# Optimization experiments

Hardware: AMD Instinct MI355X
Metric: run time of the kernel (lower is better)

Reference implementation:

```python
import jax, jax.numpy as jnp
import numpy as np

B, S, H, N, L = 256, 64, 512, 16, 2
OUT_BITS = 32            # ceil(log2(n)), n = 2**32
PTR_BITS = 6             # ceil(log2(seq_len)), seq_len = 64
OUT_DIM = 3 + PTR_BITS   # = 9
T = 2 * OUT_BITS - 1     # 63 sequential decode steps


def _ln(x, g, b):
    m = jnp.mean(x, -1, keepdims=True)
    v = jnp.mean((x - m) ** 2, -1, keepdims=True)
    return (x - m) * jax.lax.rsqrt(v + 1e-5) * g + b


def _s4_step(A, Bm, Cm, D, oW, ob, s, x):
    # diagonal-SSM S4 block step: s (B,H,N) recurrent state, x (B,H) input
    s2 = A * s + Bm * x[:, :, None]
    y = jnp.einsum('bhn,hn->bh', s2, Cm) + D * x
    y = jax.nn.gelu(y, approximate=False) @ oW + ob
    return s2, y


def _forward(input_seq, in_W, in_b, A, Bm, Cm, D, outW, outb, ln_g, ln_b, head_W, head_b):
    Bsz = input_seq.shape[0]
    dt = input_seq.dtype
    x = input_seq @ in_W + in_b            # (B,S,H)
    encoded = x                            # encoded_inputs saved before S4 stack
    # ---- encoder: L S4 blocks, residual + layernorm ----
    for j in range(L):
        def step(s, xt, j=j):
            return _s4_step(A[j], Bm[j], Cm[j], D[j], outW[j], outb[j], s, xt)
        s0 = jnp.zeros((Bsz, H, N), dt)
        _, ys = jax.lax.scan(step, s0, jnp.swapaxes(x, 0, 1))
        x = _ln(jnp.swapaxes(ys, 0, 1) + x, ln_g[j], ln_b[j])
    dec0 = jnp.broadcast_to(jnp.array([0.0, 0.0, 1.0], dt), (Bsz, 3))
    carry0 = (jnp.zeros((L, Bsz, H, N), dt), jnp.zeros((Bsz, H), dt), dec0)
    ones1 = jnp.ones((Bsz, 1), dt)

    def dstep(carry, i):
        states, ctx, dec_in = carry
        dp = dec_in @ in_W + in_b          # (B,H)
        xd = dp
        new_states = []
        for j in range(L):
            s2, y = _s4_step(A[j], Bm[j], Cm[j], D[j], outW[j], outb[j], states[j], xd)
            new_states.append(s2)
            res = jnp.where(i == 0, dp, y)   # torch code: residual=proj on step 0, else doubles x_dec
            xd = _ln(y + res, ln_g[j], ln_b[j])
        is_out = (i % 2) == 0
        # pointer retrieval (only applied on odd steps via where)
        o_ptr = jax.nn.sigmoid((xd + ctx) @ head_W + head_b)
        ptr = jnp.argmax(o_ptr[:, 3:3 + PTR_BITS], axis=1)            # (B,)
        ptr_vec = jnp.take_along_axis(encoded, ptr[:, None, None], axis=1)[:, 0]
        ctx = jnp.where(is_out, ctx, ctx + ptr_vec)
        out = jax.nn.sigmoid((xd + ctx) @ head_W + head_b)            # (B,OUT_DIM)
        next_char = jnp.where(is_out, (out[:, 0:1] > 0.5).astype(dt), jnp.zeros((Bsz, 1), dt))
        tag0 = jnp.where(is_out, 1.0, 0.0) * ones1
        tag1 = ones1 - tag0
        dec_next = jnp.concatenate([next_char, tag0, tag1], axis=1)   # (B,3)
        return (jnp.stack(new_states), ctx, dec_next), out

    _, outs = jax.lax.scan(dstep, carry0, jnp.arange(T))
    return jnp.swapaxes(outs, 0, 1)        # (B, T, OUT_DIM)


def setup_inputs() -> dict:
    ks = jax.random.split(jax.random.key(0), 8)
    f32 = jnp.float32
    return {
        'input_seq': jax.random.uniform(ks[0], (B, S, 3), f32),
        'autoregressive_steps': T,
        'in_W': jax.random.normal(ks[1], (3, H), f32) * 0.5,
        'in_b': jnp.zeros((H,), f32),
        'A': jax.random.uniform(ks[2], (L, H, N), f32, 0.5, 0.99),
        'Bm': jax.random.normal(ks[3], (L, H, N), f32) * 0.1,
        'Cm': jax.random.normal(ks[4], (L, H, N), f32) * 0.1,
        'D': jnp.ones((L, H), f32),
        'outW': jax.random.normal(ks[5], (L, H, H), f32) * 0.02,
        'outb': jnp.zeros((L, H), f32),
        'ln_g': jnp.ones((L, H), f32),
        'ln_b': jnp.zeros((L, H), f32),
        'head_W': jax.random.normal(ks[6], (H, OUT_DIM), f32) * 0.05,
        'head_b': jnp.zeros((OUT_DIM,), f32),
    }


def reference(input_seq, autoregressive_steps, in_W, in_b, A, Bm, Cm, D, outW, outb, ln_g, ln_b, head_W, head_b):
    return _forward(input_seq, in_W, in_b, A, Bm, Cm, D, outW, outb, ln_g, ln_b, head_W, head_b)
```

## Files before the change

### kernel.cpp

```cpp
#include <hip/hip_runtime.h>
#include <math.h>

#define HDIM   512
#define NDIM   16
#define SEQ    64
#define TSTEPS 63
#define BATCH  256
#define ODIM   9
#define NTHR   512


__device__ __forceinline__ float gelu_f32(float x) {
    return 0.5f * x * (1.0f + erff(x * 0.70710678118654752440f));
}

__device__ __forceinline__ float sig32(float x) {
    return 1.0f / (1.0f + expf(-x));
}

__device__ __forceinline__ void load3_l2(const float* p0, const float* p1,
                                         const float* p2,
                                         float& v0, float& v1, float& v2) {
    asm volatile(
        "global_load_dword %0, %3, off sc0\n\t"
        "global_load_dword %1, %4, off sc0\n\t"
        "global_load_dword %2, %5, off sc0\n\t"
        "s_waitcnt vmcnt(0)"
        : "=&v"(v0), "=&v"(v1), "=&v"(v2)
        : "v"(p0), "v"(p1), "v"(p2)
        : "memory");
}
__device__ __forceinline__ float load1_l2(const float* p) {
    float v;
    asm volatile("global_load_dword %0, %1, off sc0\n\t"
                 "s_waitcnt vmcnt(0)"
                 : "=v"(v) : "v"(p) : "memory");
    return v;
}

__global__ __launch_bounds__(NTHR, 2)
void s4_decode_kernel(
    const float* __restrict__ input_seq,
    const float* __restrict__ in_W,
    const float* __restrict__ in_b,
    const float* __restrict__ Aarr,
    const float* __restrict__ Barr,
    const float* __restrict__ Carr,
    const float* __restrict__ Darr,
    const float* __restrict__ outW,
    const float* __restrict__ outb,
    const float* __restrict__ ln_g,
    const float* __restrict__ ln_b,
    const float* __restrict__ headW,
    const float* __restrict__ headb,
    float* __restrict__ out,
    float* gws, float* zws,
    unsigned* fg, unsigned* fz,
    unsigned* fx, unsigned* xid)
{
    __shared__ float  ld_xd[HDIM];
    __shared__ float  ld_gall[4 * HDIM];
    __shared__ float4 ld_z4[16 * 4 * 32];
    __shared__ float  ld_D0[HDIM];
    __shared__ float  ld_D1[HDIM];
    __shared__ float  ld_red[16];
    __shared__ float  ld_hred[8 * ODIM];
    __shared__ float  ld_logit[ODIM + 1];
    __shared__ float  ld_dec[4];
    __shared__ int    ld_ptr;
    __shared__ int    ld_fast;

    const int b    = blockIdx.x;
    const int tid  = threadIdx.x;
    const int hg   = tid >> 4;
    const int n    = tid & 15;
    const int mem  = (b >> 3) & 3;
    const int gbase = b - 8 * mem;
    const int c4   = tid & 31;
    const int rg   = tid >> 5;
    const int rgE  = (rg + ((b * 5) & 15)) & 15;
    const int base_row = rgE * 32;
    const int j0 = 0 + (0 >= mem), j1 = 1 + (1 >= mem), j2 = 2 + (2 >= mem);

    unsigned myxcd;
    asm volatile("s_getreg_b32 %0, hwreg(HW_REG_XCC_ID)" : "=s"(myxcd));
    if (tid == 0) {
        __hip_atomic_store(&xid[b], myxcd, __ATOMIC_RELAXED, __HIP_MEMORY_SCOPE_AGENT);
        __hip_atomic_store(&fx[b], 1u, __ATOMIC_RELEASE, __HIP_MEMORY_SCOPE_AGENT);
        unsigned ok = 1;
        #pragma unroll
        for (int j = 0; j < 4; ++j) {
            if (j == mem) continue;
            while (__hip_atomic_load(&fx[gbase + 8 * j],
                                     __ATOMIC_ACQUIRE, __HIP_MEMORY_SCOPE_AGENT) == 0)
                __builtin_amdgcn_s_sleep(1);
            ok &= (__hip_atomic_load(&xid[gbase + 8 * j],
                                     __ATOMIC_RELAXED, __HIP_MEMORY_SCOPE_AGENT) == myxcd);
        }
        ld_fast = (int)ok;
    }

    float s0[16], s1[16];
    float A0[16], B0[16], C0[16], A1[16], B1[16], C1[16];
    #pragma unroll
    for (int k = 0; k < 16; ++k) {
        int h  = hg + 32 * k;
        int i0 = h * NDIM + n;
        int i1 = (HDIM + h) * NDIM + n;
        A0[k] = Aarr[i0]; B0[k] = Barr[i0]; C0[k] = Carr[i0];
        A1[k] = Aarr[i1]; B1[k] = Barr[i1]; C1[k] = Carr[i1];
        s0[k] = 0.f; s1[k] = 0.f;
    }

    const float inb_t = in_b[tid];
    const float w0 = in_W[tid], w1 = in_W[HDIM + tid], w2 = in_W[2 * HDIM + tid];
    const float ob0 = outb[tid], ob1 = outb[HDIM + tid];
    const float lg0 = ln_g[tid], lg1 = ln_g[HDIM + tid];
    const float lb0 = ln_b[tid], lb1 = ln_b[HDIM + tid];

    ld_D0[tid] = Darr[tid];
    ld_D1[tid] = Darr[HDIM + tid];

    const float4* Wsl = (const float4*)outW + mem * 32 + c4;

    float ctxr = 0.f;
    if (tid == 0) { ld_dec[0] = 0.f; ld_dec[1] = 0.f; ld_dec[2] = 1.f; }
    __syncthreads();
    const bool fast = (ld_fast != 0);

    for (int i = 0; i < TSTEPS; ++i) {
        float dpv = fmaf(ld_dec[0], w0, fmaf(ld_dec[1], w1, fmaf(ld_dec[2], w2, inb_t)));
        __syncthreads();
        ld_xd[tid] = dpv;
        __syncthreads();

        #pragma unroll 1
        for (int blk = 0; blk < 2; ++blk) {
            const unsigned seq = (unsigned)(2 * i + blk + 1);
            {
                float* s  = blk ? s1 : s0;
                float* Ar = blk ? A1 : A0;
                float* Br = blk ? B1 : B0;
                float* Cr = blk ? C1 : C0;
                const float* Dl = blk ? ld_D1 : ld_D0;
                #pragma unroll
                for (int k = 0; k < 16; ++k) {
                    int h = hg + 32 * k;
                    float xh = ld_xd[h];
                    float sv = fmaf(Ar[k], s[k], Br[k] * xh);
                    s[k] = sv;
                    float p = sv * Cr[k];
                    p += __shfl_xor(p, 1);
                    p += __shfl_xor(p, 2);
                    p += __shfl_xor(p, 4);
                    p += __shfl_xor(p, 8);
                    if (n == 0) ld_gall[mem * HDIM + h] = gelu_f32(p + Dl[h] * xh);
                }
            }
            __syncthreads();
            if (fast) {
                gws[b * HDIM + tid] = ld_gall[mem * HDIM + tid];
            } else {
                __hip_atomic_store(&gws[b * HDIM + tid], ld_gall[mem * HDIM + tid],
                                   __ATOMIC_RELAXED, __HIP_MEMORY_SCOPE_AGENT);
            }
            __syncthreads();
            if (tid == 4)
                __hip_atomic_store(&fg[b], seq, __ATOMIC_RELAXED, __HIP_MEMORY_SCOPE_AGENT);
            if (tid < 3) {
                int j = tid + (tid >= mem ? 1 : 0);
                while (__hip_atomic_load(&fg[gbase + 8 * j],
                                         __ATOMIC_RELAXED, __HIP_MEMORY_SCOPE_AGENT) < seq)
                    __builtin_amdgcn_s_sleep(1);
            }
            __syncthreads();
            if (fast) {
                float v0, v1, v2;
                load3_l2(&gws[(gbase + 8 * j0) * HDIM + tid],
                         &gws[(gbase + 8 * j1) * HDIM + tid],
                         &gws[(gbase + 8 * j2) * HDIM + tid], v0, v1, v2);
                ld_gall[j0 * HDIM + tid] = v0;
                ld_gall[j1 * HDIM + tid] = v1;
                ld_gall[j2 * HDIM + tid] = v2;
            } else {
                ld_gall[j0 * HDIM + tid] =
                    __hip_atomic_load(&gws[(gbase + 8 * j0) * HDIM + tid],
                                      __ATOMIC_RELAXED, __HIP_MEMORY_SCOPE_AGENT);
                ld_gall[j1 * HDIM + tid] =
                    __hip_atomic_load(&gws[(gbase + 8 * j1) * HDIM + tid],
                                      __ATOMIC_RELAXED, __HIP_MEMORY_SCOPE_AGENT);
                ld_gall[j2 * HDIM + tid] =
                    __hip_atomic_load(&gws[(gbase + 8 * j2) * HDIM + tid],
                                      __ATOMIC_RELAXED, __HIP_MEMORY_SCOPE_AGENT);
            }
            __syncthreads();
            {
                const float4* Wb = Wsl + (size_t)blk * HDIM * 128;
                float4 acc[4];
                #pragma unroll
                for (int bi = 0; bi < 4; ++bi) acc[bi] = make_float4(0.f, 0.f, 0.f, 0.f);
                float4 a0 = Wb[(size_t)(base_row)     * 128];
                float4 a1 = Wb[(size_t)(base_row + 1) * 128];
                #pragma unroll 2
                for (int rr = 0; rr < 32; rr += 4) {
                    int rB = base_row + ((rr + 2) & 31);
                    float4 b0 = Wb[(size_t)rB * 128];
                    float4 b1 = Wb[(size_t)(rB + 1) * 128];
                    {
                        int r = base_row + rr;
                        #pragma unroll
                        for (int bi = 0; bi < 4; ++bi) {
                            float g0 = ld_gall[bi * HDIM + r];
                            float g1 = ld_gall[bi * HDIM + r + 1];
                            acc[bi].x = fmaf(g1, a1.x, fmaf(g0, a0.x, acc[bi].x));
                            acc[bi].y = fmaf(g1, a1.y, fmaf(g0, a0.y, acc[bi].y));
                            acc[bi].z = fmaf(g1, a1.z, fmaf(g0, a0.z, acc[bi].z));
                            acc[bi].w = fmaf(g1, a1.w, fmaf(g0, a0.w, acc[bi].w));
                        }
                    }
                    int rA = base_row + ((rr + 4) & 31);
                    a0 = Wb[(size_t)rA * 128];
                    a1 = Wb[(size_t)(rA + 1) * 128];
                    {
                        int r = base_row + rr + 2;
                        #pragma unroll
                        for (int bi = 0; bi < 4; ++bi) {
                            float g0 = ld_gall[bi * HDIM + r];
                            float g1 = ld_gall[bi * HDIM + r + 1];
                            acc[bi].x = fmaf(g1, b1.x, fmaf(g0, b0.x, acc[bi].x));
                            acc[bi].y = fmaf(g1, b1.y, fmaf(g0, b0.y, acc[bi].y));
                            acc[bi].z = fmaf(g1, b1.z, fmaf(g0, b0.z, acc[bi].z));
                            acc[bi].w = fmaf(g1, b1.w, fmaf(g0, b0.w, acc[bi].w));
                        }
                    }
                }
                #pragma unroll
                for (int bi = 0; bi < 4; ++bi)
                    ld_z4[(rg * 4 + bi) * 32 + c4] = acc[bi];
            }
            __syncthreads();
            {
                const float* zf = (const float*)ld_z4;
                int bi2 = tid >> 7;
                int col = tid & 127;
                float zv = 0.f;
                #pragma unroll
                for (int k = 0; k < 16; ++k) zv += zf[(k * 4 + bi2) * 128 + col];
                float* zp = &zws[(gbase + 8 * bi2) * HDIM + mem * 128 + col];
                if (fast) *zp = zv;
                else __hip_atomic_store(zp, zv, __ATOMIC_RELAXED, __HIP_MEMORY_SCOPE_AGENT);
            }
            __syncthreads();
            if (tid == 4)
                __hip_atomic_store(&fz[b], seq, __ATOMIC_RELAXED, __HIP_MEMORY_SCOPE_AGENT);
            if (tid < 3) {
                int j = tid + (tid >= mem ? 1 : 0);
                while (__hip_atomic_load(&fz[gbase + 8 * j],
                                         __ATOMIC_RELAXED, __HIP_MEMORY_SCOPE_AGENT) < seq)
                    __builtin_amdgcn_s_sleep(1);
            }
            __syncthreads();
            {
                float zraw = fast ? load1_l2(&zws[b * HDIM + tid])
                                  : __hip_atomic_load(&zws[b * HDIM + tid],
                                                      __ATOMIC_RELAXED,
                                                      __HIP_MEMORY_SCOPE_AGENT);
                float z = zraw + (blk ? ob1 : ob0);
                float res = (i == 0) ? dpv : z;
                float tmp = z + res;
                float v1 = tmp, v2 = tmp * tmp;
                #pragma unroll
                for (int m = 1; m < 64; m <<= 1) {
                    v1 += __shfl_xor(v1, m);
                    v2 += __shfl_xor(v2, m);
                }
                if ((tid & 63) == 0) {
                    ld_red[2 * (tid >> 6)]     = v1;
                    ld_red[2 * (tid >> 6) + 1] = v2;
                }
                __syncthreads();
                float s1r = 0.f, s2r = 0.f;
                #pragma unroll
                for (int q = 0; q < 8; ++q) { s1r += ld_red[2*q]; s2r += ld_red[2*q+1]; }
                float mu  = s1r * (1.f / 512.f);
                float var = s2r * (1.f / 512.f) - mu * mu;
                float rs  = rsqrtf(var + 1e-5f);
                __syncthreads();
                ld_xd[tid] = (tmp - mu) * rs * (blk ? lg1 : lg0) + (blk ? lb1 : lb0);
                __syncthreads();
            }
        }

        {
            float v = ld_xd[tid] + ctxr;
            const float* w = headW + tid * ODIM;
            float p[ODIM];
            #pragma unroll
            for (int o = 0; o < ODIM; ++o) p[o] = v * w[o];
            #pragma unroll
            for (int m = 1; m < 64; m <<= 1) {
                #pragma unroll
                for (int o = 0; o < ODIM; ++o) p[o] += __shfl_xor(p[o], m);
            }
            if ((tid & 63) == 0) {
                int wv = tid >> 6;
                #pragma unroll
                for (int o = 0; o < ODIM; ++o) ld_hred[wv * ODIM + o] = p[o];
            }
            __syncthreads();
            if (tid < ODIM) {
                float s = headb[tid];
                #pragma unroll
                for (int wv = 0; wv < 8; ++wv) s += ld_hred[wv * ODIM + tid];
                ld_logit[tid] = s;
            }
            __syncthreads();
        }

        const bool is_out = ((i & 1) == 0);
        if (is_out) {
            if (tid < ODIM)
                out[(b * TSTEPS + i) * ODIM + tid] = sig32(ld_logit[tid]);
            if (tid == 0) {
                float nc = (sig32(ld_logit[0]) > 0.5f) ? 1.f : 0.f;
                ld_dec[0] = nc; ld_dec[1] = 1.f; ld_dec[2] = 0.f;
            }
            __syncthreads();
        } else {
            if (tid == 0) {
                int best = 0; float bv = sig32(ld_logit[3]);
                #pragma unroll
                for (int o = 1; o < 6; ++o) {
                    float v2 = sig32(ld_logit[3 + o]);
                    if (v2 > bv) { bv = v2; best = o; }
                }
                ld_ptr = best;
                ld_dec[0] = 0.f; ld_dec[1] = 0.f; ld_dec[2] = 1.f;
            }
            __syncthreads();
            {
                const float* iseq = input_seq + (b * SEQ + ld_ptr) * 3;
                float e0 = iseq[0], e1 = iseq[1], e2 = iseq[2];
                ctxr += fmaf(e0, w0, fmaf(e1, w1, fmaf(e2, w2, inb_t)));
            }
            __syncthreads();
            {
                float v = ld_xd[tid] + ctxr;
                const float* w = headW + tid * ODIM;
                float p[ODIM];
                #pragma unroll
                for (int o = 0; o < ODIM; ++o) p[o] = v * w[o];
                #pragma unroll
                for (int m = 1; m < 64; m <<= 1) {
                    #pragma unroll
                    for (int o = 0; o < ODIM; ++o) p[o] += __shfl_xor(p[o], m);
                }
                if ((tid & 63) == 0) {
                    int wv = tid >> 6;
                    #pragma unroll
                    for (int o = 0; o < ODIM; ++o) ld_hred[wv * ODIM + o] = p[o];
                }
                __syncthreads();
                if (tid < ODIM) {
                    float s = headb[tid];
                    #pragma unroll
                    for (int wv = 0; wv < 8; ++wv) s += ld_hred[wv * ODIM + tid];
                    out[(b * TSTEPS + i) * ODIM + tid] = sig32(s);
                }
            }
            __syncthreads();
        }
    }
}

extern "C" void kernel_launch(void* const* d_in, const int* in_sizes, int n_in,
                              void* d_out, int out_size, void* d_ws, size_t ws_size,
                              hipStream_t stream) {
    (void)in_sizes; (void)n_in; (void)ws_size; (void)out_size;
    const float* input_seq = (const float*)d_in[0];
    const float* in_W   = (const float*)d_in[2];
    const float* in_b   = (const float*)d_in[3];
    const float* Aarr   = (const float*)d_in[4];
    const float* Barr   = (const float*)d_in[5];
    const float* Carr   = (const float*)d_in[6];
    const float* Darr   = (const float*)d_in[7];
    const float* outW   = (const float*)d_in[8];
    const float* outb   = (const float*)d_in[9];
    const float* ln_g   = (const float*)d_in[10];
    const float* ln_b   = (const float*)d_in[11];
    const float* headW  = (const float*)d_in[12];
    const float* headb  = (const float*)d_in[13];
    float* out = (float*)d_out;

    unsigned* fg  = (unsigned*)d_ws;
    unsigned* fz  = fg + BATCH;
    unsigned* fx  = fz + BATCH;
    unsigned* xid = fx + BATCH;
    float* gws = (float*)((char*)d_ws + 4096);
    float* zws = gws + BATCH * HDIM;

    hipMemsetAsync(d_ws, 0, 4096, stream);

    s4_decode_kernel<<<BATCH, NTHR, 0, stream>>>(
        input_seq, in_W, in_b, Aarr, Barr, Carr, Darr,
        outW, outb, ln_g, ln_b, headW, headb, out,
        gws, zws, fg, fz, fx, xid);
}
```

Before: 1.363 ms.

## Prefetch outW rows across flag waits, vectorize LDS reads, trim barriers

Each thread now loads the first 8 outW rows of the next block's slice into registers before spinning on the cross-block z flag. The later rows are double-buffered in 4-row chunks, and the GEMV reads the gelu vector as float4 from shared memory. The gelu results are written straight to the global workspace from the state loop, which removes a separate copy phase and its barrier. The flag waits now run on a single thread, and two redundant __syncthreads are dropped. The goal is to hide weight-load latency and cut per-step synchronisation, at the cost of more register pressure and a serialised flag poll.

```diff
diff --git a/kernel.cpp b/kernel.cpp
--- a/kernel.cpp
+++ b/kernel.cpp
@@ -36,6 +36,31 @@
                  "s_waitcnt vmcnt(0)"
                  : "=v"(v) : "v"(p) : "memory");
     return v;
+}
+
+__device__ __forceinline__ void flag_barrier(unsigned* flags, int b, int gbase,
+                                             int mem, unsigned seq) {
+    __hip_atomic_store(&flags[b], seq, __ATOMIC_RELAXED, __HIP_MEMORY_SCOPE_AGENT);
+    #pragma unroll
+    for (int j = 0; j < 4; ++j) {
+        if (j == mem) continue;
+        while (__hip_atomic_load(&flags[gbase + 8 * j],
+                                 __ATOMIC_RELAXED, __HIP_MEMORY_SCOPE_AGENT) < seq)
+            __builtin_amdgcn_s_sleep(1);
+    }
+}
+
+__device__ __forceinline__ void chunk_fma(float4 w0, float4 w1, float4 w2,
+                                          float4 w3, const float4* g4p,
+                                          int idx, float4 (&acc)[4]) {
+    #pragma unroll
+    for (int bi = 0; bi < 4; ++bi) {
+        float4 gv = g4p[bi * 128 + idx];
+        acc[bi].x = fmaf(gv.x,w0.x, fmaf(gv.y,w1.x, fmaf(gv.z,w2.x, fmaf(gv.w,w3.x, acc[bi].x))));
+        acc[bi].y = fmaf(gv.x,w0.y, fmaf(gv.y,w1.y, fmaf(gv.z,w2.y, fmaf(gv.w,w3.y, acc[bi].y))));
+        acc[bi].z = fmaf(gv.x,w0.z, fmaf(gv.y,w1.z, fmaf(gv.z,w2.z, fmaf(gv.w,w3.z, acc[bi].z))));
+        acc[bi].w = fmaf(gv.x,w0.w, fmaf(gv.y,w1.w, fmaf(gv.z,w2.w, fmaf(gv.w,w3.w, acc[bi].w))));
+    }
 }
 
 __global__ __launch_bounds__(NTHR, 2)
@@ -58,9 +83,9 @@
     unsigned* fg, unsigned* fz,
     unsigned* fx, unsigned* xid)
 {
+    __shared__ float4 ld_gall4[4 * 128];
+    __shared__ float4 ld_z4[16 * 4 * 32];
     __shared__ float  ld_xd[HDIM];
-    __shared__ float  ld_gall[4 * HDIM];
-    __shared__ float4 ld_z4[16 * 4 * 32];
     __shared__ float  ld_D0[HDIM];
     __shared__ float  ld_D1[HDIM];
     __shared__ float  ld_red[16];
@@ -69,6 +94,7 @@
     __shared__ float  ld_dec[4];
     __shared__ int    ld_ptr;
     __shared__ int    ld_fast;
+    float* ld_gall = (float*)ld_gall4;
 
     const int b    = blockIdx.x;
     const int tid  = threadIdx.x;
@@ -80,6 +106,7 @@
     const int rg   = tid >> 5;
     const int rgE  = (rg + ((b * 5) & 15)) & 15;
     const int base_row = rgE * 32;
+    const int gb4  = base_row >> 2;
     const int j0 = 0 + (0 >= mem), j1 = 1 + (1 >= mem), j2 = 2 + (2 >= mem);
 
     unsigned myxcd;
@@ -128,9 +155,12 @@
     __syncthreads();
     const bool fast = (ld_fast != 0);
 
+    float4 pw[8];
+    #pragma unroll
+    for (int j = 0; j < 8; ++j) pw[j] = Wsl[(size_t)(base_row + j) * 128];
+
     for (int i = 0; i < TSTEPS; ++i) {
         float dpv = fmaf(ld_dec[0], w0, fmaf(ld_dec[1], w1, fmaf(ld_dec[2], w2, inb_t)));
-        __syncthreads();
         ld_xd[tid] = dpv;
         __syncthreads();
 
@@ -154,25 +184,17 @@
                     p += __shfl_xor(p, 2);
                     p += __shfl_xor(p, 4);
                     p += __shfl_xor(p, 8);
-                    if (n == 0) ld_gall[mem * HDIM + h] = gelu_f32(p + Dl[h] * xh);
-                }
-            }
-            __syncthreads();
-            if (fast) {
-                gws[b * HDIM + tid] = ld_gall[mem * HDIM + tid];
-            } else {
-                __hip_atomic_store(&gws[b * HDIM + tid], ld_gall[mem * HDIM + tid],
-                                   __ATOMIC_RELAXED, __HIP_MEMORY_SCOPE_AGENT);
-            }
-            __syncthreads();
-            if (tid == 4)
-                __hip_atomic_store(&fg[b], seq, __ATOMIC_RELAXED, __HIP_MEMORY_SCOPE_AGENT);
-            if (tid < 3) {
-                int j = tid + (tid >= mem ? 1 : 0);
-                while (__hip_atomic_load(&fg[gbase + 8 * j],
-                                         __ATOMIC_RELAXED, __HIP_MEMORY_SCOPE_AGENT) < seq)
-                    __builtin_amdgcn_s_sleep(1);
-            }
+                    if (n == 0) {
+                        float gv = gelu_f32(p + Dl[h] * xh);
+                        ld_gall[mem * HDIM + h] = gv;
+                        if (fast) gws[b * HDIM + h] = gv;
+                        else __hip_atomic_store(&gws[b * HDIM + h], gv,
+                                 __ATOMIC_RELAXED, __HIP_MEMORY_SCOPE_AGENT);
+                    }
+                }
+            }
+            __syncthreads();
+            if (tid == 0) flag_barrier(fg, b, gbase, mem, seq);
             __syncthreads();
             if (fast) {
                 float v0, v1, v2;
@@ -196,44 +218,31 @@
             __syncthreads();
             {
                 const float4* Wb = Wsl + (size_t)blk * HDIM * 128;
+                float4 sA[4], sB[4];
+                #pragma unroll
+                for (int j = 0; j < 4; ++j) sA[j] = Wb[(size_t)(base_row + 8 + j) * 128];
+                #pragma unroll
+                for (int j = 0; j < 4; ++j) sB[j] = Wb[(size_t)(base_row + 12 + j) * 128];
                 float4 acc[4];
                 #pragma unroll
-                for (int bi = 0; bi < 4; ++bi) acc[bi] = make_float4(0.f, 0.f, 0.f, 0.f);
-                float4 a0 = Wb[(size_t)(base_row)     * 128];
-                float4 a1 = Wb[(size_t)(base_row + 1) * 128];
-                #pragma unroll 2
-                for (int rr = 0; rr < 32; rr += 4) {
-                    int rB = base_row + ((rr + 2) & 31);
-                    float4 b0 = Wb[(size_t)rB * 128];
-                    float4 b1 = Wb[(size_t)(rB + 1) * 128];
-                    {
-                        int r = base_row + rr;
-                        #pragma unroll
-                        for (int bi = 0; bi < 4; ++bi) {
-                            float g0 = ld_gall[bi * HDIM + r];
-                            float g1 = ld_gall[bi * HDIM + r + 1];
-                            acc[bi].x = fmaf(g1, a1.x, fmaf(g0, a0.x, acc[bi].x));
-                            acc[bi].y = fmaf(g1, a1.y, fmaf(g0, a0.y, acc[bi].y));
-                            acc[bi].z = fmaf(g1, a1.z, fmaf(g0, a0.z, acc[bi].z));
-                            acc[bi].w = fmaf(g1, a1.w, fmaf(g0, a0.w, acc[bi].w));
-                        }
-                    }
-                    int rA = base_row + ((rr + 4) & 31);
-                    a0 = Wb[(size_t)rA * 128];
-                    a1 = Wb[(size_t)(rA + 1) * 128];
-                    {
-                        int r = base_row + rr + 2;
-                        #pragma unroll
-                        for (int bi = 0; bi < 4; ++bi) {
-                            float g0 = ld_gall[bi * HDIM + r];
-                            float g1 = ld_gall[bi * HDIM + r + 1];
-                            acc[bi].x = fmaf(g1, b1.x, fmaf(g0, b0.x, acc[bi].x));
-                            acc[bi].y = fmaf(g1, b1.y, fmaf(g0, b0.y, acc[bi].y));
-                            acc[bi].z = fmaf(g1, b1.z, fmaf(g0, b0.z, acc[bi].z));
-                            acc[bi].w = fmaf(g1, b1.w, fmaf(g0, b0.w, acc[bi].w));
-                        }
-                    }
-                }
+                for (int bi = 0; bi < 4; ++bi) acc[bi] = make_float4(0.f,0.f,0.f,0.f);
+                const float4* g4p = ld_gall4;
+                chunk_fma(pw[0], pw[1], pw[2], pw[3], g4p, gb4 + 0, acc);
+                chunk_fma(pw[4], pw[5], pw[6], pw[7], g4p, gb4 + 1, acc);
+                chunk_fma(sA[0], sA[1], sA[2], sA[3], g4p, gb4 + 2, acc);
+                #pragma unroll
+                for (int j = 0; j < 4; ++j) sA[j] = Wb[(size_t)(base_row + 16 + j) * 128];
+                chunk_fma(sB[0], sB[1], sB[2], sB[3], g4p, gb4 + 3, acc);
+                #pragma unroll
+                for (int j = 0; j < 4; ++j) sB[j] = Wb[(size_t)(base_row + 20 + j) * 128];
+                chunk_fma(sA[0], sA[1], sA[2], sA[3], g4p, gb4 + 4, acc);
+                #pragma unroll
+                for (int j = 0; j < 4; ++j) sA[j] = Wb[(size_t)(base_row + 24 + j) * 128];
+                chunk_fma(sB[0], sB[1], sB[2], sB[3], g4p, gb4 + 5, acc);
+                #pragma unroll
+                for (int j = 0; j < 4; ++j) sB[j] = Wb[(size_t)(base_row + 28 + j) * 128];
+                chunk_fma(sA[0], sA[1], sA[2], sA[3], g4p, gb4 + 6, acc);
+                chunk_fma(sB[0], sB[1], sB[2], sB[3], g4p, gb4 + 7, acc);
                 #pragma unroll
                 for (int bi = 0; bi < 4; ++bi)
                     ld_z4[(rg * 4 + bi) * 32 + c4] = acc[bi];
@@ -251,14 +260,12 @@
                 else __hip_atomic_store(zp, zv, __ATOMIC_RELAXED, __HIP_MEMORY_SCOPE_AGENT);
             }
             __syncthreads();
-            if (tid == 4)
-                __hip_atomic_store(&fz[b], seq, __ATOMIC_RELAXED, __HIP_MEMORY_SCOPE_AGENT);
-            if (tid < 3) {
-                int j = tid + (tid >= mem ? 1 : 0);
-                while (__hip_atomic_load(&fz[gbase + 8 * j],
-                                         __ATOMIC_RELAXED, __HIP_MEMORY_SCOPE_AGENT) < seq)
-                    __builtin_amdgcn_s_sleep(1);
-            }
+            {
+                const float4* Wn = (blk == 0) ? (Wsl + (size_t)HDIM * 128) : Wsl;
+                #pragma unroll
+                for (int j = 0; j < 8; ++j) pw[j] = Wn[(size_t)(base_row + j) * 128];
+            }
+            if (tid == 0) flag_barrier(fz, b, gbase, mem, seq);
             __syncthreads();
             {
                 float zraw = fast ? load1_l2(&zws[b * HDIM + tid])
@@ -285,7 +292,6 @@
                 float mu  = s1r * (1.f / 512.f);
                 float var = s2r * (1.f / 512.f) - mu * mu;
                 float rs  = rsqrtf(var + 1e-5f);
-                __syncthreads();
                 ld_xd[tid] = (tmp - mu) * rs * (blk ? lg1 : lg0) + (blk ? lb1 : lb0);
                 __syncthreads();
             }
```

New measurement: 2.586 ms. 1.9x slower.
